# Performance work log

Measured on AMD Instinct MI355X. Metric: run time of the kernel, lower is better.

Reference implementation:

```python
import jax, jax.numpy as jnp
import numpy as np

D_MODEL = 1024
NUM_HEADS = 16
DEPTH = D_MODEL // NUM_HEADS
NEG_BIG = -1e9


def setup_inputs() -> dict:
    key = jax.random.key(0)
    ks = jax.random.split(key, 12)
    B, S = 2, 2048
    scale = 1.0 / np.sqrt(D_MODEL)
    inp = {
        "v": jax.random.normal(ks[0], (B, S, D_MODEL), jnp.float32),
        "k": jax.random.normal(ks[1], (B, S, D_MODEL), jnp.float32),
        "q": jax.random.normal(ks[2], (B, S, D_MODEL), jnp.float32),
        "mask": jnp.zeros((B, 1, 1, S), jnp.float32),
        "Wq": jax.random.normal(ks[3], (D_MODEL, D_MODEL), jnp.float32) * scale,
        "bq": jnp.zeros((D_MODEL,), jnp.float32),
        "Wk": jax.random.normal(ks[4], (D_MODEL, D_MODEL), jnp.float32) * scale,
        "bk": jnp.zeros((D_MODEL,), jnp.float32),
        "Wv": jax.random.normal(ks[5], (D_MODEL, D_MODEL), jnp.float32) * scale,
        "bv": jnp.zeros((D_MODEL,), jnp.float32),
        "Wo": jax.random.normal(ks[6], (D_MODEL, D_MODEL), jnp.float32) * scale,
        "bo": jnp.zeros((D_MODEL,), jnp.float32),
    }
    return inp


def _split_heads(x):
    # (B, S, D) -> (B, H, S, depth)
    B, S, _ = x.shape
    return x.reshape(B, S, NUM_HEADS, DEPTH).transpose(0, 2, 1, 3)


def reference(v, k, q, mask, Wq, bq, Wk, bk, Wv, bv, Wo, bo):
    B, S, _ = q.shape
    qh = _split_heads(q @ Wq + bq)  # (B,H,Sq,depth)
    kh = _split_heads(k @ Wk + bk)  # (B,H,Sk,depth)
    vh = _split_heads(v @ Wv + bv)  # (B,H,Sk,depth)

    logits = jnp.einsum("bhqd,bhkd->bhqk", qh, kh) / jnp.sqrt(
        jnp.asarray(DEPTH, jnp.float32))
    logits = logits + mask * NEG_BIG  # mask broadcasts over heads/queries
    attn = jax.nn.softmax(logits, axis=-1)  # (B,H,Sq,Sk)
    ctx = jnp.einsum("bhqk,bhkd->bhqd", attn, vh)
    ctx = ctx.transpose(0, 2, 1, 3).reshape(B, S, D_MODEL)
    out = ctx @ Wo + bo
    return out, attn
```

## Files before the change

kernel.cpp:

```cpp
#include <hip/hip_runtime.h>
#include <stdint.h>

#define S_LEN 2048
#define DMODEL 1024
#define NHEAD 16
#define DHEAD 64
#define NBATCH 2
#define NE 4194304
#define WN 1048576

typedef unsigned short u16;
typedef float f32x16 __attribute__((ext_vector_type(16)));
typedef __bf16 bf16x8 __attribute__((ext_vector_type(8)));

__device__ __forceinline__ u16 f2bf(float x) {
  union { float f; unsigned u; } v; v.f = x;
  unsigned r = v.u + 0x7fffu + ((v.u >> 16) & 1u);
  return (u16)(r >> 16);
}
__device__ __forceinline__ unsigned cvt_pk_bf16(float lo, float hi) {
  unsigned r;
  asm("v_cvt_pk_bf16_f32 %0, %1, %2" : "=v"(r) : "v"(lo), "v"(hi));
  return r;
}
__device__ __forceinline__ void gld_lds16(const void* g, void* l) {
  __builtin_amdgcn_global_load_lds(
      (const __attribute__((address_space(1))) unsigned*)g,
      (__attribute__((address_space(3))) unsigned*)l, 16, 0, 0);
}

__global__ __launch_bounds__(256) void cvt_inputs(
    const float* __restrict__ q, const float* __restrict__ k, const float* __restrict__ v,
    u16* __restrict__ xq, u16* __restrict__ xk, u16* __restrict__ xv)
{
  int i = blockIdx.x * 256 + threadIdx.x;
  const int stride = gridDim.x * 256;
  for (; i < NE / 4; i += stride) {
    float4 a = ((const float4*)q)[i];
    float4 b = ((const float4*)k)[i];
    float4 c = ((const float4*)v)[i];
    ushort4 oa, ob, oc;
    oa.x = f2bf(a.x); oa.y = f2bf(a.y); oa.z = f2bf(a.z); oa.w = f2bf(a.w);
    ob.x = f2bf(b.x); ob.y = f2bf(b.y); ob.z = f2bf(b.z); ob.w = f2bf(b.w);
    oc.x = f2bf(c.x); oc.y = f2bf(c.y); oc.z = f2bf(c.z); oc.w = f2bf(c.w);
    ((ushort4*)xq)[i] = oa;
    ((ushort4*)xk)[i] = ob;
    ((ushort4*)xv)[i] = oc;
  }
}

__global__ __launch_bounds__(256) void wtrans(
    const float* __restrict__ Wq, const float* __restrict__ Wk,
    const float* __restrict__ Wv, const float* __restrict__ Wo,
    u16* __restrict__ oq, u16* __restrict__ ok, u16* __restrict__ ov, u16* __restrict__ oo)
{
  __shared__ u16 t[64][65];
  const float* W; u16* O;
  if (blockIdx.z == 0)      { W = Wq; O = oq; }
  else if (blockIdx.z == 1) { W = Wk; O = ok; }
  else if (blockIdx.z == 2) { W = Wv; O = ov; }
  else                      { W = Wo; O = oo; }
  const int tid = threadIdx.x;
  const int r0 = blockIdx.y * 64, c0 = blockIdx.x * 64;
#pragma unroll
  for (int i = 0; i < 4; ++i) {
    const int row = i * 16 + (tid >> 4);
    const int col = (tid & 15) * 4;
    float4 wv = *(const float4*)(W + (size_t)(r0 + row) * DMODEL + c0 + col);
    t[row][col + 0] = f2bf(wv.x);
    t[row][col + 1] = f2bf(wv.y);
    t[row][col + 2] = f2bf(wv.z);
    t[row][col + 3] = f2bf(wv.w);
  }
  __syncthreads();
#pragma unroll
  for (int i = 0; i < 4; ++i) {
    const int row = i * 16 + (tid >> 4);
    const int col = (tid & 15) * 4;
    ushort4 o;
    o.x = t[col + 0][row]; o.y = t[col + 1][row];
    o.z = t[col + 2][row]; o.w = t[col + 3][row];
    *(ushort4*)(O + (size_t)(c0 + row) * DMODEL + r0 + col) = o;
  }
}

template <int OUTMODE>
__device__ __forceinline__ void gemm_core(
    const u16* __restrict__ A, const u16* __restrict__ Bt,
    const float* __restrict__ bias, void* __restrict__ outp,
    float scale, int m0, int n0)
{
  __shared__ u16 As[128 * 32];
  __shared__ u16 Bs[128 * 32];
  const int tid = threadIdx.x;
  const int lane = tid & 63, w = tid >> 6;
  const int q_l = lane & 31, hi = lane >> 5;
  const int wr = w >> 1, wc = w & 1;

  f32x16 acc[2][2];
#pragma unroll
  for (int a = 0; a < 2; ++a)
#pragma unroll
    for (int b = 0; b < 2; ++b)
#pragma unroll
      for (int r = 0; r < 16; ++r) acc[a][b][r] = 0.f;

  const u16* srcA = A + (size_t)(m0 + (tid >> 2)) * DMODEL + (tid & 3) * 8;
  const u16* srcB = Bt + (size_t)(n0 + (tid >> 2)) * DMODEL + (tid & 3) * 8;
  u16* dstA = As + w * 512;
  u16* dstB = Bs + w * 512;

  for (int kt = 0; kt < DMODEL; kt += 32) {
    gld_lds16(srcA + kt, dstA);
    gld_lds16(srcA + kt + (size_t)64 * DMODEL, dstA + 2048);
    gld_lds16(srcB + kt, dstB);
    gld_lds16(srcB + kt + (size_t)64 * DMODEL, dstB + 2048);
    __syncthreads();
#pragma unroll
    for (int kk = 0; kk < 2; ++kk) {
      bf16x8 af[2], bfv[2];
#pragma unroll
      for (int mb = 0; mb < 2; ++mb)
        af[mb] = *reinterpret_cast<const bf16x8*>(&As[(wr * 64 + mb * 32 + q_l) * 32 + kk * 16 + hi * 8]);
#pragma unroll
      for (int nb = 0; nb < 2; ++nb)
        bfv[nb] = *reinterpret_cast<const bf16x8*>(&Bs[(wc * 64 + nb * 32 + q_l) * 32 + kk * 16 + hi * 8]);
#pragma unroll
      for (int mb = 0; mb < 2; ++mb)
#pragma unroll
        for (int nb = 0; nb < 2; ++nb)
          acc[mb][nb] = __builtin_amdgcn_mfma_f32_32x32x16_bf16(af[mb], bfv[nb], acc[mb][nb], 0, 0, 0);
    }
    __syncthreads();
  }

#pragma unroll
  for (int mb = 0; mb < 2; ++mb) {
#pragma unroll
    for (int nb = 0; nb < 2; ++nb) {
      const int n = n0 + wc * 64 + nb * 32 + q_l;
      const float bn = bias[n];
#pragma unroll
      for (int r = 0; r < 16; ++r) {
        const int m = m0 + wr * 64 + mb * 32 + (r & 3) + 8 * (r >> 2) + 4 * hi;
        const float val = (acc[mb][nb][r] + bn) * scale;
        if (OUTMODE == 0) {
          const int bb = m >> 11, s = m & 2047, hh = n >> 6, d = n & 63;
          ((u16*)outp)[(((size_t)(bb * NHEAD + hh)) * S_LEN + s) * DHEAD + d] = f2bf(val);
        } else {
          ((float*)outp)[(size_t)m * DMODEL + n] = val;
        }
      }
    }
  }
}

__global__ __launch_bounds__(256) void gemm_qkv(
    const u16* __restrict__ xq, const u16* __restrict__ xk, const u16* __restrict__ xv,
    const u16* __restrict__ wqt, const u16* __restrict__ wkt, const u16* __restrict__ wvt,
    const float* __restrict__ bq, const float* __restrict__ bk, const float* __restrict__ bv,
    u16* __restrict__ qh, u16* __restrict__ kh, u16* __restrict__ vh)
{
  const u16 *A, *Bt; const float* bias; u16* O; float scale;
  if (blockIdx.z == 0)      { A = xq; Bt = wqt; bias = bq; O = qh; scale = 0.125f; }
  else if (blockIdx.z == 1) { A = xk; Bt = wkt; bias = bk; O = kh; scale = 1.f; }
  else                      { A = xv; Bt = wvt; bias = bv; O = vh; scale = 1.f; }
  gemm_core<0>(A, Bt, bias, O, scale, blockIdx.y * 128, blockIdx.x * 128);
}

__global__ __launch_bounds__(256) void gemm_out(
    const u16* __restrict__ ctx, const u16* __restrict__ wot,
    const float* __restrict__ bo, float* __restrict__ out)
{
  gemm_core<1>(ctx, wot, bo, out, 1.f, blockIdx.y * 128, blockIdx.x * 128);
}

__global__ __launch_bounds__(256) void vtrans(const u16* __restrict__ vh, u16* __restrict__ vt)
{
  __shared__ u16 t[64][72];
  const int tid = threadIdx.x;
  const int bh = blockIdx.y;
  const int s0 = blockIdx.x * 64;
  const u16* src = vh + (size_t)bh * S_LEN * DHEAD;
  u16* dst = vt + (size_t)bh * DHEAD * S_LEN;
#pragma unroll
  for (int i = 0; i < 2; ++i) {
    const int row = i * 32 + (tid >> 3);
    const int c8 = (tid & 7) * 8;
    *(uint4*)&t[row][c8] = *(const uint4*)(src + (size_t)(s0 + row) * DHEAD + c8);
  }
  __syncthreads();
#pragma unroll
  for (int i = 0; i < 2; ++i) {
    const int d = i * 32 + (tid >> 3);
    const int c8 = (tid & 7) * 8;
    unsigned p0 = (unsigned)t[c8 + 0][d] | ((unsigned)t[c8 + 1][d] << 16);
    unsigned p1 = (unsigned)t[c8 + 2][d] | ((unsigned)t[c8 + 3][d] << 16);
    unsigned p2 = (unsigned)t[c8 + 4][d] | ((unsigned)t[c8 + 5][d] << 16);
    unsigned p3 = (unsigned)t[c8 + 6][d] | ((unsigned)t[c8 + 7][d] << 16);
    uint4 o; o.x = p0; o.y = p1; o.z = p2; o.w = p3;
    *(uint4*)(dst + (size_t)d * S_LEN + s0 + c8) = o;
  }
}

__global__ __launch_bounds__(256) void attn_pv(
    const u16* __restrict__ qh, const u16* __restrict__ kh,
    const u16* __restrict__ vt, const float* __restrict__ mask,
    float* __restrict__ inv_g, u16* __restrict__ ctx_out)
{
  __shared__ float smaskv[S_LEN];

  const int tid = threadIdx.x;
  const int lane = tid & 63, w = tid >> 6;
  const int q_l = lane & 31, hi = lane >> 5;
  const int qb = blockIdx.x, bh = blockIdx.y;
  const int b = bh >> 4, h = bh & 15;
  const int q0 = qb * 128 + w * 32;

  const u16* Qp = qh + (size_t)bh * S_LEN * DHEAD;
  const u16* Kp = kh + (size_t)bh * S_LEN * DHEAD;
  const u16* Vp = vt + (size_t)bh * DHEAD * S_LEN;

  for (int i = tid; i < S_LEN / 4; i += 256) {
    float4 m4 = ((const float4*)(mask + (size_t)b * S_LEN))[i];
    smaskv[4 * i + 0] = m4.x * -1e9f;
    smaskv[4 * i + 1] = m4.y * -1e9f;
    smaskv[4 * i + 2] = m4.z * -1e9f;
    smaskv[4 * i + 3] = m4.w * -1e9f;
  }
  __syncthreads();

  bf16x8 qf[4];
  {
    const u16* qrow = Qp + (size_t)(q0 + q_l) * DHEAD + hi * 8;
#pragma unroll
    for (int c = 0; c < 4; ++c) qf[c] = *reinterpret_cast<const bf16x8*>(qrow + c * 16);
  }

  float rsum = 0.f;
  f32x16 cacc[2];
#pragma unroll
  for (int db = 0; db < 2; ++db)
#pragma unroll
    for (int r = 0; r < 16; ++r) cacc[db][r] = 0.f;

  bf16x8 kc[4], kn[4];
  {
    const u16* kr0 = Kp + (size_t)q_l * DHEAD + hi * 8;
#pragma unroll
    for (int c = 0; c < 4; ++c) kc[c] = *reinterpret_cast<const bf16x8*>(kr0 + c * 16);
  }

#pragma unroll 2
  for (int t = 0; t < 64; ++t) {
    const int k0 = t * 32;
    if (t < 63) {
      const u16* krow = Kp + (size_t)(k0 + 32 + q_l) * DHEAD + hi * 8;
#pragma unroll
      for (int c = 0; c < 4; ++c) kn[c] = *reinterpret_cast<const bf16x8*>(krow + c * 16);
    }
    bf16x8 vf[2][2];
#pragma unroll
    for (int s2 = 0; s2 < 2; ++s2)
#pragma unroll
      for (int db = 0; db < 2; ++db)
        vf[s2][db] = *reinterpret_cast<const bf16x8*>(
            Vp + (size_t)(db * 32 + q_l) * S_LEN + k0 + s2 * 16 + hi * 8);
    f32x16 a0, a1;
#pragma unroll
    for (int r = 0; r < 16; ++r) { a0[r] = 0.f; a1[r] = 0.f; }
    a0 = __builtin_amdgcn_mfma_f32_32x32x16_bf16(kc[0], qf[0], a0, 0, 0, 0);
    a0 = __builtin_amdgcn_mfma_f32_32x32x16_bf16(kc[1], qf[1], a0, 0, 0, 0);
    a1 = __builtin_amdgcn_mfma_f32_32x32x16_bf16(kc[2], qf[2], a1, 0, 0, 0);
    a1 = __builtin_amdgcn_mfma_f32_32x32x16_bf16(kc[3], qf[3], a1, 0, 0, 0);

    float p[16];
#pragma unroll
    for (int g = 0; g < 4; ++g) {
      const float4 mk = *(const float4*)&smaskv[k0 + 8 * g + 4 * hi];
      p[4 * g + 0] = __expf(a0[4 * g + 0] + a1[4 * g + 0] + mk.x);
      p[4 * g + 1] = __expf(a0[4 * g + 1] + a1[4 * g + 1] + mk.y);
      p[4 * g + 2] = __expf(a0[4 * g + 2] + a1[4 * g + 2] + mk.z);
      p[4 * g + 3] = __expf(a0[4 * g + 3] + a1[4 * g + 3] + mk.w);
      rsum += (p[4 * g + 0] + p[4 * g + 1]) + (p[4 * g + 2] + p[4 * g + 3]);
    }
    unsigned pk[8];
#pragma unroll
    for (int g = 0; g < 4; ++g) {
      pk[2 * g + 0] = cvt_pk_bf16(p[4 * g + 0], p[4 * g + 1]);
      pk[2 * g + 1] = cvt_pk_bf16(p[4 * g + 2], p[4 * g + 3]);
    }
#pragma unroll
    for (int s2 = 0; s2 < 2; ++s2) {
      unsigned a0u = pk[4 * s2 + 0], b0u = pk[4 * s2 + 2];
      unsigned a1u = pk[4 * s2 + 1], b1u = pk[4 * s2 + 3];
      asm volatile("v_permlane32_swap_b32 %0, %1" : "+v"(a0u), "+v"(b0u));
      asm volatile("v_permlane32_swap_b32 %0, %1" : "+v"(a1u), "+v"(b1u));
      uint4 frw; frw.x = a0u; frw.y = a1u; frw.z = b0u; frw.w = b1u;
      bf16x8 pa = __builtin_bit_cast(bf16x8, frw);
#pragma unroll
      for (int db = 0; db < 2; ++db)
        cacc[db] = __builtin_amdgcn_mfma_f32_32x32x16_bf16(pa, vf[s2][db], cacc[db], 0, 0, 0);
    }
#pragma unroll
    for (int c = 0; c < 4; ++c) kc[c] = kn[c];
  }

  rsum += __shfl_xor(rsum, 32, 64);
  const float inv = 1.0f / rsum;
  if (lane < 32) inv_g[(size_t)bh * S_LEN + q0 + lane] = inv;

  float sc[16];
#pragma unroll
  for (int r = 0; r < 16; ++r)
    sc[r] = __shfl(inv, (r & 3) + 8 * (r >> 2) + 4 * hi, 64);
#pragma unroll
  for (int db = 0; db < 2; ++db)
#pragma unroll
    for (int r = 0; r < 16; ++r) {
      const int qq = (r & 3) + 8 * (r >> 2) + 4 * hi;
      ctx_out[((size_t)(b * S_LEN + q0 + qq)) * DMODEL + h * DHEAD + db * 32 + q_l] =
          f2bf(cacc[db][r] * sc[r]);
    }
}

__global__ __launch_bounds__(256) void attn_store(
    const u16* __restrict__ qh, const u16* __restrict__ kh,
    const float* __restrict__ mask, const float* __restrict__ inv_g,
    float* __restrict__ attn_out)
{
  const int tid = threadIdx.x;
  const int lane = tid & 63, w = tid >> 6;
  const int q_l = lane & 31, hi = lane >> 5;
  const int qb = blockIdx.x, bh = blockIdx.y;
  const int b = bh >> 4;
  const int q0 = qb * 32;

  const u16* Qp = qh + (size_t)bh * S_LEN * DHEAD;
  const u16* Kp = kh + (size_t)bh * S_LEN * DHEAD;

  bf16x8 qf[4];
  {
    const u16* qrow = Qp + (size_t)(q0 + q_l) * DHEAD + hi * 8;
#pragma unroll
    for (int c = 0; c < 4; ++c) qf[c] = *reinterpret_cast<const bf16x8*>(qrow + c * 16);
  }

  float myinv[16];
#pragma unroll
  for (int r = 0; r < 16; ++r)
    myinv[r] = inv_g[(size_t)bh * S_LEN + q0 + (r & 3) + 8 * (r >> 2) + 4 * hi];

  const int k0w = w * 512;
  float mval[16];
#pragma unroll
  for (int t = 0; t < 16; ++t)
    mval[t] = mask[(size_t)b * S_LEN + k0w + t * 32 + q_l] * -1e9f;

  float* base = attn_out + ((size_t)bh * S_LEN + q0 + 4 * hi) * S_LEN + k0w + q_l;

  bf16x8 kc[4], kn[4];
  {
    const u16* kr0 = Kp + (size_t)(k0w + q_l) * DHEAD + hi * 8;
#pragma unroll
    for (int c = 0; c < 4; ++c) kc[c] = *reinterpret_cast<const bf16x8*>(kr0 + c * 16);
  }

#pragma unroll
  for (int t = 0; t < 16; ++t) {
    if (t < 15) {
      const u16* krow = Kp + (size_t)(k0w + (t + 1) * 32 + q_l) * DHEAD + hi * 8;
#pragma unroll
      for (int c = 0; c < 4; ++c) kn[c] = *reinterpret_cast<const bf16x8*>(krow + c * 16);
    }
    f32x16 a0, a1;
#pragma unroll
    for (int r = 0; r < 16; ++r) { a0[r] = 0.f; a1[r] = 0.f; }
    a0 = __builtin_amdgcn_mfma_f32_32x32x16_bf16(qf[0], kc[0], a0, 0, 0, 0);
    a0 = __builtin_amdgcn_mfma_f32_32x32x16_bf16(qf[1], kc[1], a0, 0, 0, 0);
    a1 = __builtin_amdgcn_mfma_f32_32x32x16_bf16(qf[2], kc[2], a1, 0, 0, 0);
    a1 = __builtin_amdgcn_mfma_f32_32x32x16_bf16(qf[3], kc[3], a1, 0, 0, 0);
#pragma unroll
    for (int r = 0; r < 16; ++r) {
      const float pv = __expf(a0[r] + a1[r] + mval[t]) * myinv[r];
      const int rr = (r & 3) + 8 * (r >> 2);
      base[(size_t)rr * S_LEN + t * 32] = pv;
    }
#pragma unroll
    for (int c = 0; c < 4; ++c) kc[c] = kn[c];
  }
}

extern "C" void kernel_launch(void* const* d_in, const int* in_sizes, int n_in,
                              void* d_out, int out_size, void* d_ws, size_t ws_size,
                              hipStream_t stream)
{
  (void)in_sizes; (void)n_in; (void)out_size; (void)ws_size;
  const float* v    = (const float*)d_in[0];
  const float* k    = (const float*)d_in[1];
  const float* q    = (const float*)d_in[2];
  const float* mask = (const float*)d_in[3];
  const float* Wq   = (const float*)d_in[4];
  const float* bq   = (const float*)d_in[5];
  const float* Wk   = (const float*)d_in[6];
  const float* bk   = (const float*)d_in[7];
  const float* Wv   = (const float*)d_in[8];
  const float* bv   = (const float*)d_in[9];
  const float* Wo   = (const float*)d_in[10];
  const float* bo   = (const float*)d_in[11];

  u16* ws16 = (u16*)d_ws;
  u16* xq  = ws16;
  u16* xk  = ws16 + (size_t)1 * NE;
  u16* xv  = ws16 + (size_t)2 * NE;
  u16* qh  = ws16 + (size_t)3 * NE;
  u16* kh  = ws16 + (size_t)4 * NE;
  u16* vh  = ws16 + (size_t)5 * NE;
  u16* wqt = ws16 + (size_t)6 * NE;
  u16* wkt = wqt + WN;
  u16* wvt = wkt + WN;
  u16* wot = wvt + WN;
  float* inv_g = (float*)(wot + WN);
  u16* vt  = xq;
  u16* ctx = xk;

  float* outp  = (float*)d_out;
  float* attnp = outp + (size_t)NE;

  cvt_inputs<<<dim3(1024), dim3(256), 0, stream>>>(q, k, v, xq, xk, xv);
  wtrans<<<dim3(16, 16, 4), dim3(256), 0, stream>>>(Wq, Wk, Wv, Wo, wqt, wkt, wvt, wot);
  gemm_qkv<<<dim3(8, 32, 3), dim3(256), 0, stream>>>(xq, xk, xv, wqt, wkt, wvt,
                                                     bq, bk, bv, qh, kh, vh);
  vtrans<<<dim3(32, 32), dim3(256), 0, stream>>>(vh, vt);
  attn_pv<<<dim3(16, 32), dim3(256), 0, stream>>>(qh, kh, vt, mask, inv_g, ctx);
  attn_store<<<dim3(64, 32), dim3(256), 0, stream>>>(qh, kh, mask, inv_g, attnp);
  gemm_out<<<dim3(8, 32), dim3(256), 0, stream>>>(ctx, wot, bo, outp);
}
```

Before: 360.5 us.

## Split attention into single-wave blocks, prefetch V, fuse output GEMM with attn store

attn_pv now runs one 64-thread wave per block with a swizzled 1D grid that spreads heads across blocks. It reads the mask straight from global memory instead of staging it in shared memory, and it double-buffers V fragments alongside K. The output projection GEMM and the attention-probability store kernel are merged into one launch, with the first 256 blocks doing the GEMM and the rest writing attn. The aim is better occupancy and overlap of the GEMM with the bandwidth-heavy attn write, and one fewer launch. The cost is more register pressure from the V prefetch and per-iteration global mask loads.

```diff
diff --git a/kernel.cpp b/kernel.cpp
--- a/kernel.cpp
+++ b/kernel.cpp
@@ -168,13 +168,6 @@
   gemm_core<0>(A, Bt, bias, O, scale, blockIdx.y * 128, blockIdx.x * 128);
 }
 
-__global__ __launch_bounds__(256) void gemm_out(
-    const u16* __restrict__ ctx, const u16* __restrict__ wot,
-    const float* __restrict__ bo, float* __restrict__ out)
-{
-  gemm_core<1>(ctx, wot, bo, out, 1.f, blockIdx.y * 128, blockIdx.x * 128);
-}
-
 __global__ __launch_bounds__(256) void vtrans(const u16* __restrict__ vh, u16* __restrict__ vt)
 {
   __shared__ u16 t[64][72];
@@ -203,32 +196,23 @@
   }
 }
 
-__global__ __launch_bounds__(256) void attn_pv(
+__global__ __launch_bounds__(64) void attn_pv(
     const u16* __restrict__ qh, const u16* __restrict__ kh,
     const u16* __restrict__ vt, const float* __restrict__ mask,
     float* __restrict__ inv_g, u16* __restrict__ ctx_out)
 {
-  __shared__ float smaskv[S_LEN];
-
-  const int tid = threadIdx.x;
-  const int lane = tid & 63, w = tid >> 6;
+  const int lane = threadIdx.x;
   const int q_l = lane & 31, hi = lane >> 5;
-  const int qb = blockIdx.x, bh = blockIdx.y;
+  const int id = blockIdx.x;
+  const int bh = (id & 7) | (((id >> 3) & 3) << 3);
+  const int qb = id >> 5;
   const int b = bh >> 4, h = bh & 15;
-  const int q0 = qb * 128 + w * 32;
+  const int q0 = qb * 32;
 
   const u16* Qp = qh + (size_t)bh * S_LEN * DHEAD;
   const u16* Kp = kh + (size_t)bh * S_LEN * DHEAD;
   const u16* Vp = vt + (size_t)bh * DHEAD * S_LEN;
-
-  for (int i = tid; i < S_LEN / 4; i += 256) {
-    float4 m4 = ((const float4*)(mask + (size_t)b * S_LEN))[i];
-    smaskv[4 * i + 0] = m4.x * -1e9f;
-    smaskv[4 * i + 1] = m4.y * -1e9f;
-    smaskv[4 * i + 2] = m4.z * -1e9f;
-    smaskv[4 * i + 3] = m4.w * -1e9f;
-  }
-  __syncthreads();
+  const float* mrow = mask + (size_t)b * S_LEN;
 
   bf16x8 qf[4];
   {
@@ -244,11 +228,17 @@
 #pragma unroll
     for (int r = 0; r < 16; ++r) cacc[db][r] = 0.f;
 
-  bf16x8 kc[4], kn[4];
+  bf16x8 kc[4], kn[4], vc[2][2], vn[2][2];
   {
     const u16* kr0 = Kp + (size_t)q_l * DHEAD + hi * 8;
 #pragma unroll
     for (int c = 0; c < 4; ++c) kc[c] = *reinterpret_cast<const bf16x8*>(kr0 + c * 16);
+#pragma unroll
+    for (int s2 = 0; s2 < 2; ++s2)
+#pragma unroll
+      for (int db = 0; db < 2; ++db)
+        vc[s2][db] = *reinterpret_cast<const bf16x8*>(
+            Vp + (size_t)(db * 32 + q_l) * S_LEN + s2 * 16 + hi * 8);
   }
 
 #pragma unroll 2
@@ -258,14 +248,13 @@
       const u16* krow = Kp + (size_t)(k0 + 32 + q_l) * DHEAD + hi * 8;
 #pragma unroll
       for (int c = 0; c < 4; ++c) kn[c] = *reinterpret_cast<const bf16x8*>(krow + c * 16);
-    }
-    bf16x8 vf[2][2];
-#pragma unroll
-    for (int s2 = 0; s2 < 2; ++s2)
-#pragma unroll
-      for (int db = 0; db < 2; ++db)
-        vf[s2][db] = *reinterpret_cast<const bf16x8*>(
-            Vp + (size_t)(db * 32 + q_l) * S_LEN + k0 + s2 * 16 + hi * 8);
+#pragma unroll
+      for (int s2 = 0; s2 < 2; ++s2)
+#pragma unroll
+        for (int db = 0; db < 2; ++db)
+          vn[s2][db] = *reinterpret_cast<const bf16x8*>(
+              Vp + (size_t)(db * 32 + q_l) * S_LEN + k0 + 32 + s2 * 16 + hi * 8);
+    }
     f32x16 a0, a1;
 #pragma unroll
     for (int r = 0; r < 16; ++r) { a0[r] = 0.f; a1[r] = 0.f; }
@@ -277,11 +266,11 @@
     float p[16];
 #pragma unroll
     for (int g = 0; g < 4; ++g) {
-      const float4 mk = *(const float4*)&smaskv[k0 + 8 * g + 4 * hi];
-      p[4 * g + 0] = __expf(a0[4 * g + 0] + a1[4 * g + 0] + mk.x);
-      p[4 * g + 1] = __expf(a0[4 * g + 1] + a1[4 * g + 1] + mk.y);
-      p[4 * g + 2] = __expf(a0[4 * g + 2] + a1[4 * g + 2] + mk.z);
-      p[4 * g + 3] = __expf(a0[4 * g + 3] + a1[4 * g + 3] + mk.w);
+      const float4 mk = *(const float4*)&mrow[k0 + 8 * g + 4 * hi];
+      p[4 * g + 0] = __expf(a0[4 * g + 0] + a1[4 * g + 0] + mk.x * -1e9f);
+      p[4 * g + 1] = __expf(a0[4 * g + 1] + a1[4 * g + 1] + mk.y * -1e9f);
+      p[4 * g + 2] = __expf(a0[4 * g + 2] + a1[4 * g + 2] + mk.z * -1e9f);
+      p[4 * g + 3] = __expf(a0[4 * g + 3] + a1[4 * g + 3] + mk.w * -1e9f);
       rsum += (p[4 * g + 0] + p[4 * g + 1]) + (p[4 * g + 2] + p[4 * g + 3]);
     }
     unsigned pk[8];
@@ -300,10 +289,14 @@
       bf16x8 pa = __builtin_bit_cast(bf16x8, frw);
 #pragma unroll
       for (int db = 0; db < 2; ++db)
-        cacc[db] = __builtin_amdgcn_mfma_f32_32x32x16_bf16(pa, vf[s2][db], cacc[db], 0, 0, 0);
+        cacc[db] = __builtin_amdgcn_mfma_f32_32x32x16_bf16(pa, vc[s2][db], cacc[db], 0, 0, 0);
     }
 #pragma unroll
     for (int c = 0; c < 4; ++c) kc[c] = kn[c];
+#pragma unroll
+    for (int s2 = 0; s2 < 2; ++s2)
+#pragma unroll
+      for (int db = 0; db < 2; ++db) vc[s2][db] = vn[s2][db];
   }
 
   rsum += __shfl_xor(rsum, 32, 64);
@@ -324,15 +317,24 @@
     }
 }
 
-__global__ __launch_bounds__(256) void attn_store(
+__global__ __launch_bounds__(256) void tail_fused(
+    const u16* __restrict__ ctx, const u16* __restrict__ wot, const float* __restrict__ bo,
+    float* __restrict__ out,
     const u16* __restrict__ qh, const u16* __restrict__ kh,
     const float* __restrict__ mask, const float* __restrict__ inv_g,
     float* __restrict__ attn_out)
 {
+  if (blockIdx.x < 256) {
+    const int gid = blockIdx.x;
+    gemm_core<1>(ctx, wot, bo, out, 1.f, (gid >> 3) * 128, (gid & 7) * 128);
+    return;
+  }
+  const int id = blockIdx.x - 256;
   const int tid = threadIdx.x;
   const int lane = tid & 63, w = tid >> 6;
   const int q_l = lane & 31, hi = lane >> 5;
-  const int qb = blockIdx.x, bh = blockIdx.y;
+  const int bh = (id & 7) | (((id >> 3) & 3) << 3);
+  const int qb = id >> 5;
   const int b = bh >> 4;
   const int q0 = qb * 32;
 
@@ -432,7 +434,7 @@
   gemm_qkv<<<dim3(8, 32, 3), dim3(256), 0, stream>>>(xq, xk, xv, wqt, wkt, wvt,
                                                      bq, bk, bv, qh, kh, vh);
   vtrans<<<dim3(32, 32), dim3(256), 0, stream>>>(vh, vt);
-  attn_pv<<<dim3(16, 32), dim3(256), 0, stream>>>(qh, kh, vt, mask, inv_g, ctx);
-  attn_store<<<dim3(64, 32), dim3(256), 0, stream>>>(qh, kh, mask, inv_g, attnp);
-  gemm_out<<<dim3(8, 32), dim3(256), 0, stream>>>(ctx, wot, bo, outp);
-}
+  attn_pv<<<dim3(2048), dim3(64), 0, stream>>>(qh, kh, vt, mask, inv_g, ctx);
+  tail_fused<<<dim3(2304), dim3(256), 0, stream>>>(ctx, wot, bo, outp,
+                                                   qh, kh, mask, inv_g, attnp);
+}
```

New measurement: 328.7 us. 8.8% less time.
